# Optimization experiments

Measured on AMD Instinct MI355X. Metric: run time of the kernel, lower is better.

Reference implementation:

```python
import jax, jax.numpy as jnp
import numpy as np

BIG = 1e6  # sentinel 'no zero pixel found yet' distance; BIG**2 = 1e12 fits fp32


def _edt(is_fg):
    """Exact Euclidean distance transform (scipy.distance_transform_edt semantics):
    distance from each nonzero pixel to the nearest zero pixel. is_fg: [N,H,W] bool.
    Separable exact algorithm: 1D vertical distance-to-zero per column via cummax
    scans, then min-plus convolution with the parabola (j-k)^2 along rows."""
    N, H, W = is_fg.shape
    is_zero = ~is_fg
    ih = jnp.arange(H, dtype=jnp.float32)[None, :, None]
    # nearest zero at-or-above / at-or-below along H (per column)
    up = jax.lax.cummax(jnp.where(is_zero, ih, -BIG), axis=1)
    dn = -jax.lax.cummax(jnp.where(is_zero, -ih, -BIG), axis=1, reverse=True)
    g = jnp.minimum(ih - up, dn - ih)               # [N,H,W] vertical 1D distance
    g2 = jnp.minimum(g, BIG) ** 2
    ks = jnp.arange(W, dtype=jnp.float32)
    def col(j):
        # exact 2D squared distance for output column j: min_k (j-k)^2 + g(.,.,k)^2
        return jnp.min((j.astype(jnp.float32) - ks) ** 2 + g2, axis=-1)  # [N,H]
    d2 = jax.lax.map(col, jnp.arange(W))            # [W,N,H], sequential -> low memory
    return jnp.sqrt(jnp.moveaxis(d2, 0, -1))        # [N,H,W]


def setup_inputs() -> dict:
    key = jax.random.key(0)
    k1, k2 = jax.random.split(key)
    B, C, H, W = 8, 12, 256, 256
    logits = jax.random.normal(k1, (B, C, H, W), dtype=jnp.float32)
    targets = jax.random.randint(k2, (B, H, W), 0, C, dtype=jnp.int32)
    return {"logits": logits, "targets": targets}


def reference(logits, targets):
    B, C, H, W = logits.shape
    probs = jax.nn.softmax(logits, axis=1)                                  # [B,C,H,W]
    gt = targets[:, None, :, :] == jnp.arange(C, dtype=targets.dtype)[None, :, None, None]
    m = gt.reshape(B * C, H, W)
    pos = _edt(m)          # distance inside foreground to nearest background
    neg = _edt(~m)         # distance inside background to nearest foreground
    dt = (neg - pos).reshape(B, C, H, W)
    has_fg = gt.any(axis=(2, 3))                                            # [B,C]
    dt = jnp.where(has_fg[:, :, None, None], dt, 0.0)
    # per-image, per-class min-max normalization (matches torch view(B,-1).min/max)
    dmin = dt.min(axis=(2, 3), keepdims=True)
    dmax = dt.max(axis=(2, 3), keepdims=True)
    dt = (dt - dmin) / (dmax - dmin + 1e-8)
    inter = jnp.sum(probs * dt, axis=(2, 3))                                # [B,C]
    denom = jnp.sum(probs * probs, axis=(2, 3)) + jnp.sum(dt * dt, axis=(2, 3)) + 1e-6
    dice = 2.0 * inter / denom
    # sum_c mean_b (1-dice) / C  == mean over (b,c) since ignore_index=255 is out of range
    return jnp.mean(1.0 - dice)
```

## Files before the change

### kernel.cpp

```cpp
#include <hip/hip_runtime.h>
#include <math.h>

constexpr int B_  = 8;
constexpr int C_  = 12;
constexpr int H_  = 256;
constexpr int W_  = 256;
constexpr int HW_ = H_ * W_;
constexpr int NBC_ = B_ * C_;
constexpr int VB_  = NBC_ * 8;
constexpr int SMB_ = B_ * (HW_ / 512);
constexpr int PADL_ = 128;
constexpr int LROW_ = PADL_ + W_ + PADL_;


__global__ void __launch_bounds__(512) k_vert(
                     const int* __restrict__ t,
                     unsigned short* __restrict__ gpk,
                     int* __restrict__ hasfg_p,
                     float* __restrict__ out) {
    int tid = threadIdx.x;
    if (blockIdx.x == 0 && tid == 0) out[0] = 0.0f;
    constexpr int SEG = 16, SH = 16;
    int s  = tid >> 5;
    int wl = tid & 31;
    int blk = blockIdx.x;
    int bc = blk >> 3;
    int w0 = (blk & 7) * 32;
    int b = bc / C_, c = bc - b * C_;
    int w = w0 + wl;
    const int* base = t + b * HW_ + w;
    int h0 = s * SH;

    unsigned tp[SH / 4];
    int lastEq = -1, lastNeq = -1, firstEq = 256, firstNeq = 256;
    #pragma unroll
    for (int i = 0; i < SH; ++i) {
        int tv = base[(h0 + i) * W_];
        if ((i & 3) == 0) tp[i >> 2] = 0;
        tp[i >> 2] |= (unsigned)tv << ((i & 3) * 8);
        int h = h0 + i;
        if (tv == c) { lastEq = h;  if (firstEq  == 256) firstEq  = h; }
        else         { lastNeq = h; if (firstNeq == 256) firstNeq = h; }
    }
    __shared__ int sLE[SEG][32], sLN[SEG][32], sFE[SEG][32], sFN[SEG][32];
    sLE[s][wl] = lastEq; sLN[s][wl] = lastNeq;
    sFE[s][wl] = firstEq; sFN[s][wl] = firstNeq;
    __syncthreads();

    int carLE = -1, carLN = -1;
    for (int q = 0; q < s; ++q) {
        carLE = max(carLE, sLE[q][wl]);
        carLN = max(carLN, sLN[q][wl]);
    }
    int carFE = 256, carFN = 256;
    for (int q = s + 1; q < SEG; ++q) {
        carFE = min(carFE, sFE[q][wl]);
        carFN = min(carFN, sFN[q][wl]);
    }

    bool pred = false;
    if (tid < 32) {
        int m = -1;
        #pragma unroll
        for (int q = 0; q < SEG; ++q) m = max(m, sLE[q][tid]);
        pred = (m >= 0);
    }
    bool anyfg = __any(pred);
    if (tid == 0) hasfg_p[blk] = anyfg ? 1 : 0;

    unsigned ap[SH / 4];
    {
        int le = carLE, ln = carLN;
        #pragma unroll
        for (int i = 0; i < SH; ++i) {
            int h = h0 + i;
            int tv = (tp[i >> 2] >> ((i & 3) * 8)) & 0xFF;
            int lz;
            if (tv == c) { le = h; lz = ln; } else { ln = h; lz = le; }
            unsigned a = (lz < 0) ? 255u : (unsigned)(h - lz - 1);
            if ((i & 3) == 0) ap[i >> 2] = 0;
            ap[i >> 2] |= a << ((i & 3) * 8);
        }
    }
    {
        int fe = carFE, fn = carFN;
        unsigned short* gk = gpk + (size_t)bc * HW_ + w;
        #pragma unroll
        for (int i = SH - 1; i >= 0; --i) {
            int h = h0 + i;
            int tv = (tp[i >> 2] >> ((i & 3) * 8)) & 0xFF;
            int nz; bool fg;
            if (tv == c) { fe = h; fg = true;  nz = fn; }
            else         { fn = h; fg = false; nz = fe; }
            unsigned au = (ap[i >> 2] >> ((i & 3) * 8)) & 0xFF;
            int dl  = (au == 255u) ? 0x7FFF : (int)au + 1;
            int dnx = (nz > 255) ? 0x7FFF : (nz - h);
            int d = min(dl, dnx);
            gk[h * W_] = (unsigned short)(d | (fg ? 0x8000 : 0));
        }
    }
}

__global__ void __launch_bounds__(256) k_sm(
                     const float* __restrict__ logits,
                     float2* __restrict__ den) {
    int tid = threadIdx.x;
    int pb = blockIdx.x;
    int b = pb >> 7;
    int p = ((pb & 127) << 9) + tid * 2;
    const float* lb = logits + (size_t)b * C_ * HW_ + p;
    float2 l[C_];
    float mxx = -3.4e38f, mxy = -3.4e38f;
    #pragma unroll
    for (int c = 0; c < C_; ++c) {
        l[c] = *(const float2*)(lb + (size_t)c * HW_);
        mxx = fmaxf(mxx, l[c].x);
        mxy = fmaxf(mxy, l[c].y);
    }
    float sx = 0.f, sy = 0.f;
    #pragma unroll
    for (int c = 0; c < C_; ++c) {
        sx += __expf(l[c].x - mxx);
        sy += __expf(l[c].y - mxy);
    }
    *(float4*)(den + (size_t)b * HW_ + p) =
        make_float4(mxx, 1.0f / sx, mxy, 1.0f / sy);
}

__global__ void __launch_bounds__(256) k_edt(
                      const unsigned short* __restrict__ gpk,
                      const float* __restrict__ logits,
                      const float2* __restrict__ den,
                      const int* __restrict__ hasfg_p,
                      float* __restrict__ part) {
    __shared__ float sp[4][LROW_];
    __shared__ float sn[4][LROW_];
    int wave = threadIdx.x >> 6;
    int lane = threadIdx.x & 63;
    int row = blockIdx.x * 4 + wave;
    int bc = row >> 8;
    int b = bc / C_, c = bc - b * C_;
    int h = row & (H_ - 1);

    int hfl = 0;
    if (lane < 8) hfl = hasfg_p[bc * 8 + lane];
    bool hf = __any(hfl != 0);

    const float*  lrow = logits + ((size_t)b * C_ + c) * HW_ + h * W_;
    const float2* drow = den + (size_t)b * HW_ + h * W_;
    float lv[4]; float2 mv[4];
    #pragma unroll
    for (int i = 0; i < 4; ++i) {
        int j = lane + 64 * i;
        lv[i] = lrow[j];
        mv[i] = drow[j];
    }

    float dv[4];
    if (hf) {
        const ushort4 v4 = ((const ushort4*)(gpk + (size_t)row * W_))[lane];

        float4 inf4 = make_float4(3.0e38f, 3.0e38f, 3.0e38f, 3.0e38f);
        int slot = (lane < 32) ? lane : (lane + 64);
        ((float4*)&sp[wave][0])[slot] = inf4;
        ((float4*)&sn[wave][0])[slot] = inf4;

        float s1 = (float)(1000000 - h);
        float sent2 = s1 * s1;
        float4 fpv, fnv;
        {
            const unsigned short* vs = (const unsigned short*)&v4;
            float* fp = (float*)&fpv;
            float* fn = (float*)&fnv;
            #pragma unroll
            for (int q = 0; q < 4; ++q) {
                unsigned v = vs[q];
                unsigned d = v & 0x7FFFu;
                float g2 = (d == 0x7FFFu) ? sent2 : (float)(d * d);
                bool fg = (v & 0x8000u) != 0;
                fp[q] = fg ? g2 : 0.0f;
                fn[q] = fg ? 0.0f : g2;
            }
        }
        ((float4*)&sp[wave][PADL_])[lane] = fpv;
        ((float4*)&sn[wave][PADL_])[lane] = fnv;
        asm volatile("s_waitcnt lgkmcnt(0)" ::: "memory");

        float bp[4], bn[4];
        #pragma unroll
        for (int i = 0; i < 4; ++i) {
            int j = PADL_ + lane + 64 * i;
            bp[i] = sp[wave][j];
            bn[i] = sn[wave][j];
        }
        {
            bool doneN = false;
            int r = 1;
            for (; r <= PADL_; ++r) {
                float fr = (float)r;
                float r2 = fr * fr;
                float m = fmaxf(fmaxf(bn[0], bn[1]), fmaxf(bn[2], bn[3]));
                if (!__any(r2 < m)) { doneN = true; break; }
                #pragma unroll
                for (int i = 0; i < 4; ++i) {
                    int j = PADL_ + lane + 64 * i;
                    float v = fminf(sn[wave][j - r], sn[wave][j + r]);
                    bn[i] = fminf(bn[i], fmaf(fr, fr, v));
                }
            }
            if (!doneN) {
                for (; r < W_; ++r) {
                    float fr = (float)r;
                    float r2 = fr * fr;
                    float m = fmaxf(fmaxf(bn[0], bn[1]), fmaxf(bn[2], bn[3]));
                    if (!__any(r2 < m)) break;
                    #pragma unroll
                    for (int i = 0; i < 4; ++i) {
                        int j = PADL_ + lane + 64 * i;
                        int jm = max(j - r, 0);
                        int jp = min(j + r, LROW_ - 1);
                        float v = fminf(sn[wave][jm], sn[wave][jp]);
                        bn[i] = fminf(bn[i], fmaf(fr, fr, v));
                    }
                }
            }
        }
        {
            bool doneP = false;
            int r = 1;
            for (; r <= PADL_; ++r) {
                float fr = (float)r;
                float r2 = fr * fr;
                float m = fmaxf(fmaxf(bp[0], bp[1]), fmaxf(bp[2], bp[3]));
                if (!__any(r2 < m)) { doneP = true; break; }
                #pragma unroll
                for (int i = 0; i < 4; ++i) {
                    int j = PADL_ + lane + 64 * i;
                    float v = fminf(sp[wave][j - r], sp[wave][j + r]);
                    bp[i] = fminf(bp[i], fmaf(fr, fr, v));
                }
            }
            if (!doneP) {
                for (; r < W_; ++r) {
                    float fr = (float)r;
                    float r2 = fr * fr;
                    float m = fmaxf(fmaxf(bp[0], bp[1]), fmaxf(bp[2], bp[3]));
                    if (!__any(r2 < m)) break;
                    #pragma unroll
                    for (int i = 0; i < 4; ++i) {
                        int j = PADL_ + lane + 64 * i;
                        int jm = max(j - r, 0);
                        int jp = min(j + r, LROW_ - 1);
                        float v = fminf(sp[wave][jm], sp[wave][jp]);
                        bp[i] = fminf(bp[i], fmaf(fr, fr, v));
                    }
                }
            }
        }
        #pragma unroll
        for (int i = 0; i < 4; ++i) dv[i] = sqrtf(bn[i]) - sqrtf(bp[i]);
    } else {
        #pragma unroll
        for (int i = 0; i < 4; ++i) dv[i] = 0.0f;
    }

    float s_pd = 0.f, s_p = 0.f, s_pp = 0.f, s_d = 0.f, s_dd = 0.f;
    float mn = 3.4e38f, mx = -3.4e38f;
    #pragma unroll
    for (int i = 0; i < 4; ++i) {
        float2 mi = mv[i];
        float pr = __expf(lv[i] - mi.x) * mi.y;
        float d = dv[i];
        s_pd = fmaf(pr, d, s_pd);
        s_p += pr;
        s_pp = fmaf(pr, pr, s_pp);
        s_d += d;
        s_dd = fmaf(d, d, s_dd);
        mn = fminf(mn, d);
        mx = fmaxf(mx, d);
    }
    #pragma unroll
    for (int off = 32; off; off >>= 1) {
        s_pd += __shfl_down(s_pd, off);
        s_p  += __shfl_down(s_p, off);
        s_pp += __shfl_down(s_pp, off);
        s_d  += __shfl_down(s_d, off);
        s_dd += __shfl_down(s_dd, off);
        mn = fminf(mn, __shfl_down(mn, off));
        mx = fmaxf(mx, __shfl_down(mx, off));
    }
    if (lane == 0) {
        float4* p4 = (float4*)(part + (size_t)row * 8);
        p4[0] = make_float4(s_pd, s_p, s_pp, s_d);
        p4[1] = make_float4(s_dd, mn, mx, 0.0f);
    }
}

__global__ void __launch_bounds__(256) k_bcred(
                       const float* __restrict__ part, float* __restrict__ out) {
    int bc = blockIdx.x;
    int tid = threadIdx.x;
    const float4* p4 = (const float4*)(part + ((size_t)bc * 256 + tid) * 8);
    float4 a = p4[0], bq = p4[1];
    float s_pd = a.x, s_p = a.y, s_pp = a.z;
    float s_d = a.w, s_dd = bq.x, mn = bq.y, mx = bq.z;
    #pragma unroll
    for (int off = 32; off; off >>= 1) {
        s_pd += __shfl_down(s_pd, off);
        s_p  += __shfl_down(s_p, off);
        s_pp += __shfl_down(s_pp, off);
        s_d  += __shfl_down(s_d, off);
        s_dd += __shfl_down(s_dd, off);
        mn = fminf(mn, __shfl_down(mn, off));
        mx = fmaxf(mx, __shfl_down(mx, off));
    }
    __shared__ float red[4][7];
    int wave = tid >> 6, lane = tid & 63;
    if (lane == 0) {
        red[wave][0] = s_pd; red[wave][1] = s_p; red[wave][2] = s_pp;
        red[wave][3] = s_d;  red[wave][4] = s_dd; red[wave][5] = mn; red[wave][6] = mx;
    }
    __syncthreads();
    if (tid == 0) {
        s_pd = red[0][0]; s_p = red[0][1]; s_pp = red[0][2];
        s_d = red[0][3]; s_dd = red[0][4]; mn = red[0][5]; mx = red[0][6];
        for (int w = 1; w < 4; ++w) {
            s_pd += red[w][0]; s_p += red[w][1]; s_pp += red[w][2];
            s_d += red[w][3]; s_dd += red[w][4];
            mn = fminf(mn, red[w][5]); mx = fmaxf(mx, red[w][6]);
        }
        float sc = 1.0f / (mx - mn + 1e-8f);
        float inter = sc * (s_pd - mn * s_p);
        float d2 = sc * sc * (s_dd - 2.0f * mn * s_d + mn * mn * (float)HW_);
        float dice = 2.0f * inter / (s_pp + d2 + 1e-6f);
        atomicAdd(out, (1.0f - dice) * (1.0f / (float)NBC_));
    }
}

extern "C" void kernel_launch(void* const* d_in, const int* in_sizes, int n_in,
                              void* d_out, int out_size, void* d_ws, size_t ws_size,
                              hipStream_t stream) {
    const float* logits  = (const float*)d_in[0];
    const int*   targets = (const int*)d_in[1];
    float* out = (float*)d_out;

    unsigned short* gpk = (unsigned short*)d_ws;
    int* hasfg_p = (int*)(gpk + (size_t)NBC_ * HW_);
    float* part = (float*)(hasfg_p + NBC_ * 8);
    float2* den = (float2*)(part + (size_t)NBC_ * H_ * 8);

    k_vert<<<VB_, 512, 0, stream>>>(targets, gpk, hasfg_p, out);
    k_sm<<<SMB_, 256, 0, stream>>>(logits, den);
    k_edt<<<NBC_ * H_ / 4, 256, 0, stream>>>(gpk, logits, den, hasfg_p, part);
    k_bcred<<<NBC_, 256, 0, stream>>>(part, out);
}
```

Measured before the change: 106.4 us.

## Merge softmax into vertical-scan kernel and store full probabilities

```diff
diff --git a/kernel.cpp b/kernel.cpp
--- a/kernel.cpp
+++ b/kernel.cpp
@@ -8,17 +8,49 @@
 constexpr int HW_ = H_ * W_;
 constexpr int NBC_ = B_ * C_;
 constexpr int VB_  = NBC_ * 8;
-constexpr int SMB_ = B_ * (HW_ / 512);
+constexpr int SMB_ = B_ * (HW_ / 1024);
 constexpr int PADL_ = 128;
 constexpr int LROW_ = PADL_ + W_ + PADL_;
 
 
-__global__ void __launch_bounds__(512) k_vert(
+__global__ void __launch_bounds__(512) k_vs(
                      const int* __restrict__ t,
+                     const float* __restrict__ logits,
                      unsigned short* __restrict__ gpk,
                      int* __restrict__ hasfg_p,
+                     float* __restrict__ probs,
                      float* __restrict__ out) {
     int tid = threadIdx.x;
+    if (blockIdx.x >= VB_) {
+        int pb = blockIdx.x - VB_;
+        int b = pb >> 6;
+        int p = ((pb & 63) << 10) + tid * 2;
+        const float* lb = logits + (size_t)b * C_ * HW_ + p;
+        float2 l[C_];
+        float mxx = -3.4e38f, mxy = -3.4e38f;
+        #pragma unroll
+        for (int c = 0; c < C_; ++c) {
+            l[c] = *(const float2*)(lb + (size_t)c * HW_);
+            mxx = fmaxf(mxx, l[c].x);
+            mxy = fmaxf(mxy, l[c].y);
+        }
+        float sx = 0.f, sy = 0.f;
+        #pragma unroll
+        for (int c = 0; c < C_; ++c) {
+            l[c].x = __expf(l[c].x - mxx);
+            l[c].y = __expf(l[c].y - mxy);
+            sx += l[c].x;
+            sy += l[c].y;
+        }
+        float ix = 1.0f / sx, iy = 1.0f / sy;
+        float* pbp = probs + (size_t)b * C_ * HW_ + p;
+        #pragma unroll
+        for (int c = 0; c < C_; ++c) {
+            *(float2*)(pbp + (size_t)c * HW_) = make_float2(l[c].x * ix, l[c].y * iy);
+        }
+        return;
+    }
+
     if (blockIdx.x == 0 && tid == 0) out[0] = 0.0f;
     constexpr int SEG = 16, SH = 16;
     int s  = tid >> 5;
@@ -101,36 +133,9 @@
     }
 }
 
-__global__ void __launch_bounds__(256) k_sm(
-                     const float* __restrict__ logits,
-                     float2* __restrict__ den) {
-    int tid = threadIdx.x;
-    int pb = blockIdx.x;
-    int b = pb >> 7;
-    int p = ((pb & 127) << 9) + tid * 2;
-    const float* lb = logits + (size_t)b * C_ * HW_ + p;
-    float2 l[C_];
-    float mxx = -3.4e38f, mxy = -3.4e38f;
-    #pragma unroll
-    for (int c = 0; c < C_; ++c) {
-        l[c] = *(const float2*)(lb + (size_t)c * HW_);
-        mxx = fmaxf(mxx, l[c].x);
-        mxy = fmaxf(mxy, l[c].y);
-    }
-    float sx = 0.f, sy = 0.f;
-    #pragma unroll
-    for (int c = 0; c < C_; ++c) {
-        sx += __expf(l[c].x - mxx);
-        sy += __expf(l[c].y - mxy);
-    }
-    *(float4*)(den + (size_t)b * HW_ + p) =
-        make_float4(mxx, 1.0f / sx, mxy, 1.0f / sy);
-}
-
 __global__ void __launch_bounds__(256) k_edt(
                       const unsigned short* __restrict__ gpk,
-                      const float* __restrict__ logits,
-                      const float2* __restrict__ den,
+                      const float* __restrict__ probs,
                       const int* __restrict__ hasfg_p,
                       float* __restrict__ part) {
     __shared__ float sp[4][LROW_];
@@ -139,22 +144,16 @@
     int lane = threadIdx.x & 63;
     int row = blockIdx.x * 4 + wave;
     int bc = row >> 8;
-    int b = bc / C_, c = bc - b * C_;
     int h = row & (H_ - 1);
 
     int hfl = 0;
     if (lane < 8) hfl = hasfg_p[bc * 8 + lane];
     bool hf = __any(hfl != 0);
 
-    const float*  lrow = logits + ((size_t)b * C_ + c) * HW_ + h * W_;
-    const float2* drow = den + (size_t)b * HW_ + h * W_;
-    float lv[4]; float2 mv[4];
-    #pragma unroll
-    for (int i = 0; i < 4; ++i) {
-        int j = lane + 64 * i;
-        lv[i] = lrow[j];
-        mv[i] = drow[j];
-    }
+    const float* prow = probs + (size_t)bc * HW_ + h * W_;
+    float pv[4];
+    #pragma unroll
+    for (int i = 0; i < 4; ++i) pv[i] = prow[lane + 64 * i];
 
     float dv[4];
     if (hf) {
@@ -268,8 +267,7 @@
     float mn = 3.4e38f, mx = -3.4e38f;
     #pragma unroll
     for (int i = 0; i < 4; ++i) {
-        float2 mi = mv[i];
-        float pr = __expf(lv[i] - mi.x) * mi.y;
+        float pr = pv[i];
         float d = dv[i];
         s_pd = fmaf(pr, d, s_pd);
         s_p += pr;
@@ -347,10 +345,10 @@
     unsigned short* gpk = (unsigned short*)d_ws;
     int* hasfg_p = (int*)(gpk + (size_t)NBC_ * HW_);
     float* part = (float*)(hasfg_p + NBC_ * 8);
-    float2* den = (float2*)(part + (size_t)NBC_ * H_ * 8);
-
-    k_vert<<<VB_, 512, 0, stream>>>(targets, gpk, hasfg_p, out);
-    k_sm<<<SMB_, 256, 0, stream>>>(logits, den);
-    k_edt<<<NBC_ * H_ / 4, 256, 0, stream>>>(gpk, logits, den, hasfg_p, part);
+    float* probs = part + (size_t)NBC_ * H_ * 8;
+
+    k_vs<<<VB_ + SMB_, 512, 0, stream>>>(targets, logits, gpk,
+                                         hasfg_p, probs, out);
+    k_edt<<<NBC_ * H_ / 4, 256, 0, stream>>>(gpk, probs, hasfg_p, part);
     k_bcred<<<NBC_, 256, 0, stream>>>(part, out);
 }
```

After: 104.8 us. Within noise of the previous version (-1.5%).
